# Performance work log

Hardware: AMD Instinct MI355X
Metric: run time of the kernel (lower is better)

The kernel has to match this reference:

```python
import jax, jax.numpy as jnp
import numpy as np

B, H, W, C = 16, 56, 56, 512
HEADS, WS, SHIFT = 16, 7, 3
N = WS * WS            # tokens per window = 49
NW = (H // WS) * (W // WS)  # 64 windows per image
HID = 4 * C
EPS = 1e-5


def _rel_pos_index():
    coords = np.stack(np.meshgrid(np.arange(WS), np.arange(WS), indexing='ij'))  # (2,WS,WS)
    coords = coords.reshape(2, -1)                       # (2,N)
    rel = coords[:, :, None] - coords[:, None, :]        # (2,N,N)
    rel = rel.transpose(1, 2, 0).astype(np.int64)        # (N,N,2)
    rel[:, :, 0] += WS - 1
    rel[:, :, 1] += WS - 1
    rel[:, :, 0] *= 2 * WS - 1
    return rel.sum(-1)                                   # (N,N) in [0, (2WS-1)^2)


def _attn_mask():
    # standard Swin shifted-window mask
    img = np.zeros((H, W), dtype=np.int64)
    cnt = 0
    for hs in (slice(0, -WS), slice(-WS, -SHIFT), slice(-SHIFT, None)):
        for ws in (slice(0, -WS), slice(-WS, -SHIFT), slice(-SHIFT, None)):
            img[hs, ws] = cnt
            cnt += 1
    win = img.reshape(H // WS, WS, W // WS, WS).transpose(0, 2, 1, 3).reshape(NW, N)
    diff = win[:, None, :] - win[:, :, None]             # (NW,N,N)
    return np.where(diff != 0, -100.0, 0.0).astype(np.float32)


REL_IDX = _rel_pos_index()
MASK = _attn_mask()


def _ln(x, g, b):
    m = x.mean(-1, keepdims=True)
    v = ((x - m) ** 2).mean(-1, keepdims=True)
    return (x - m) * jax.lax.rsqrt(v + EPS) * g + b


def setup_inputs() -> dict:
    key = jax.random.key(0)
    ks = jax.random.split(key, 16)
    s = 0.02
    return {
        'x': jax.random.normal(ks[0], (B, H * W, C), jnp.float32),
        'norm1_g': jnp.ones((C,), jnp.float32),
        'norm1_b': jnp.zeros((C,), jnp.float32),
        'qkv_w': jax.random.normal(ks[1], (3 * C, C), jnp.float32) * s,
        'qkv_b': jnp.zeros((3 * C,), jnp.float32),
        'proj_w': jax.random.normal(ks[2], (C, C), jnp.float32) * s,
        'proj_b': jnp.zeros((C,), jnp.float32),
        'rpb': jax.random.normal(ks[3], ((2 * WS - 1) ** 2, HEADS), jnp.float32) * s,
        'norm2_g': jnp.ones((C,), jnp.float32),
        'norm2_b': jnp.zeros((C,), jnp.float32),
        'fc1_w': jax.random.normal(ks[4], (HID, C), jnp.float32) * s,
        'fc1_b': jnp.zeros((HID,), jnp.float32),
        'fc2_w': jax.random.normal(ks[5], (C, HID), jnp.float32) * s,
        'fc2_b': jnp.zeros((C,), jnp.float32),
    }


def reference(x, norm1_g, norm1_b, qkv_w, qkv_b, proj_w, proj_b, rpb,
              norm2_g, norm2_b, fc1_w, fc1_b, fc2_w, fc2_b):
    hd = C // HEADS
    scale = hd ** -0.5

    shortcut = x
    h = _ln(x, norm1_g, norm1_b).reshape(B, H, W, C)
    # cyclic shift
    h = jnp.roll(h, (-SHIFT, -SHIFT), axis=(1, 2))
    # window partition -> (B*NW, N, C)
    h = h.reshape(B, H // WS, WS, W // WS, WS, C).transpose(0, 1, 3, 2, 4, 5)
    h = h.reshape(B * NW, N, C)

    qkv = h @ qkv_w.T + qkv_b                            # (B*NW, N, 3C)
    qkv = qkv.reshape(B * NW, N, 3, HEADS, hd).transpose(2, 0, 3, 1, 4)
    q, k, v = qkv[0], qkv[1], qkv[2]                     # (B*NW, HEADS, N, hd)

    attn = jnp.einsum('whnd,whmd->whnm', q * scale, k)   # (B*NW, HEADS, N, N)
    bias = rpb[REL_IDX].transpose(2, 0, 1)               # (HEADS, N, N)
    attn = attn + bias[None]
    attn = attn.reshape(B, NW, HEADS, N, N) + jnp.asarray(MASK)[None, :, None]
    attn = jax.nn.softmax(attn.reshape(B * NW, HEADS, N, N), axis=-1)

    out = jnp.einsum('whnm,whmd->whnd', attn, v)         # (B*NW, HEADS, N, hd)
    out = out.transpose(0, 2, 1, 3).reshape(B * NW, N, C)
    out = out @ proj_w.T + proj_b

    # window reverse + reverse shift
    out = out.reshape(B, H // WS, W // WS, WS, WS, C).transpose(0, 1, 3, 2, 4, 5)
    out = out.reshape(B, H, W, C)
    out = jnp.roll(out, (SHIFT, SHIFT), axis=(1, 2)).reshape(B, H * W, C)

    x = shortcut + out
    m = _ln(x, norm2_g, norm2_b)
    m = jax.nn.gelu(m @ fc1_w.T + fc1_b, approximate=False) @ fc2_w.T + fc2_b
    return x + m
```

## Files before the change

### kernel.cpp

```cpp
#include <hip/hip_runtime.h>
#include <hip/hip_bf16.h>

typedef __bf16 bf16;
typedef __bf16 bf16x8 __attribute__((ext_vector_type(8)));
typedef __bf16 bf16x4 __attribute__((ext_vector_type(4)));
typedef __bf16 bf16x2 __attribute__((ext_vector_type(2)));
typedef float f32x4 __attribute__((ext_vector_type(4)));

#define M_TOK 50176

#define GLD16(dst, src) __builtin_amdgcn_global_load_lds( \
    (const __attribute__((address_space(1))) void*)(src), \
    (__attribute__((address_space(3))) void*)(dst), 16, 0, 0)

__global__ __launch_bounds__(256) void convert_w_kernel(
    const float* __restrict__ w0, const float* __restrict__ w1,
    const float* __restrict__ w2, const float* __restrict__ w3,
    bf16* __restrict__ dst)
{
    int blk = blockIdx.x;
    const float* src; size_t srel, drel;
    if (blk < 768)       { src = w0; srel = (size_t)blk * 1024;          drel = srel; }
    else if (blk < 1024) { src = w1; srel = (size_t)(blk - 768) * 1024;  drel = 786432 + srel; }
    else if (blk < 2048) { src = w2; srel = (size_t)(blk - 1024) * 1024; drel = 1048576 + srel; }
    else                 { src = w3; srel = (size_t)(blk - 2048) * 1024; drel = 2097152 + srel; }
    int i = threadIdx.x * 4;
    float4 v = *(const float4*)(src + srel + i);
    bf16* d = dst + drel + i;
    d[0] = (bf16)v.x; d[1] = (bf16)v.y; d[2] = (bf16)v.z; d[3] = (bf16)v.w;
}

__global__ __launch_bounds__(64) void bias_table_kernel(
    const float* __restrict__ rpb, float* __restrict__ bt)
{
    int tq = blockIdx.x;
    int type = tq / 784, r = tq - type * 784;
    int head = r / 49, q = r - head * 49;
    int k = threadIdx.x;
    float v;
    if (k < 49) {
        int yq = q / 7, xq = q - yq * 7;
        int yk = k / 7, xk = k - yk * 7;
        int ridx = (yq - yk + 6) * 13 + (xq - xk + 6);
        v = rpb[ridx * 16 + head];
        int th = type >> 1, tw = type & 1;
        int qid = 3 * (th ? (yq < 4 ? 1 : 2) : 0) + (tw ? (xq < 4 ? 1 : 2) : 0);
        int kid = 3 * (th ? (yk < 4 ? 1 : 2) : 0) + (tw ? (xk < 4 ? 1 : 2) : 0);
        if (qid != kid) v -= 100.f;
    } else {
        v = -1e9f;
    }
    bt[(size_t)tq * 64 + k] = v;
}

__global__ __launch_bounds__(256) void ln1_window_kernel(
    const float* __restrict__ x, const float* __restrict__ g, const float* __restrict__ bta,
    bf16* __restrict__ h)
{
    int t = blockIdx.x;
    int win = t / 49, n = t - win * 49;
    int bi = win >> 6, nw = win & 63;
    int wh = nw >> 3, ww = nw & 7;
    int ny = n / 7, nx = n - ny * 7;
    int r = wh * 7 + ny + 3; if (r >= 56) r -= 56;
    int c = ww * 7 + nx + 3; if (c >= 56) c -= 56;
    const float* xr = x + ((size_t)bi * 3136 + r * 56 + c) * 512;
    int tid = threadIdx.x;
    float v0 = xr[tid];
    float v1 = xr[tid + 256];
    float s = v0 + v1, ss = v0 * v0 + v1 * v1;
#pragma unroll
    for (int o = 32; o; o >>= 1) { s += __shfl_down(s, o, 64); ss += __shfl_down(ss, o, 64); }
    __shared__ float red[8];
    int wave = tid >> 6, lane = tid & 63;
    if (lane == 0) { red[wave] = s; red[4 + wave] = ss; }
    __syncthreads();
    float S = red[0] + red[1] + red[2] + red[3];
    float SS = red[4] + red[5] + red[6] + red[7];
    float mean = S * (1.f / 512.f);
    float var = SS * (1.f / 512.f) - mean * mean;
    float rstd = rsqrtf(var + 1e-5f);
    bf16* hr = h + (size_t)t * 512;
    hr[tid] = (bf16)((v0 - mean) * rstd * g[tid] + bta[tid]);
    hr[tid + 256] = (bf16)((v1 - mean) * rstd * g[tid + 256] + bta[tid + 256]);
}

template <int X1BF>
__global__ __launch_bounds__(256) void ln2_kernel(
    const void* __restrict__ x1, const float* __restrict__ g,
    const float* __restrict__ bta, bf16* __restrict__ outp)
{
    int t = blockIdx.x;
    int tid = threadIdx.x;
    float v0, v1;
    if constexpr (X1BF) {
        const bf16* xr = (const bf16*)x1 + (size_t)t * 512;
        v0 = (float)xr[tid]; v1 = (float)xr[tid + 256];
    } else {
        const float* xr = (const float*)x1 + (size_t)t * 512;
        v0 = xr[tid]; v1 = xr[tid + 256];
    }
    float s = v0 + v1, ss = v0 * v0 + v1 * v1;
#pragma unroll
    for (int o = 32; o; o >>= 1) { s += __shfl_down(s, o, 64); ss += __shfl_down(ss, o, 64); }
    __shared__ float red[8];
    int wave = tid >> 6, lane = tid & 63;
    if (lane == 0) { red[wave] = s; red[4 + wave] = ss; }
    __syncthreads();
    float S = red[0] + red[1] + red[2] + red[3];
    float SS = red[4] + red[5] + red[6] + red[7];
    float mean = S * (1.f / 512.f);
    float var = SS * (1.f / 512.f) - mean * mean;
    float rstd = rsqrtf(var + 1e-5f);
    bf16* hr = outp + (size_t)t * 512;
    hr[tid] = (bf16)((v0 - mean) * rstd * g[tid] + bta[tid]);
    hr[tid + 256] = (bf16)((v1 - mean) * rstd * g[tid + 256] + bta[tid + 256]);
}

template <int MODE, int K, int X1BF>
__global__ __launch_bounds__(256, 4) void gemm128b_kernel(
    const bf16* __restrict__ A, const bf16* __restrict__ Wt, const float* __restrict__ bias,
    void* __restrict__ outp, const void* __restrict__ extra, int N)
{
    __shared__ bf16 As[128][64];
    __shared__ bf16 Ws[128][64];
    constexpr int NT = K / 64;
    int gx = gridDim.x;
    int lin = blockIdx.y * gx + blockIdx.x;
    int q8 = (gx * gridDim.y) >> 3;
    int lin2 = (lin & 7) * q8 + (lin >> 3);
    int bn = lin2 % gx, bm = lin2 / gx;
    int tid = threadIdx.x;
    int w = tid >> 6, lane = tid & 63;
    int wm = w >> 1, wn = w & 1;
    int fr = lane & 15, fq = lane >> 4;
    int srow = lane >> 3;
    int scol = ((lane & 7) ^ srow) * 8;
    const bf16* gA = A + (size_t)(bm * 128 + w * 32 + srow) * K + scol;
    const bf16* gB = Wt + (size_t)(bn * 128 + w * 32 + srow) * K + scol;

    f32x4 acc[4][4];
    f32x4 z = {0.f, 0.f, 0.f, 0.f};
#pragma unroll
    for (int mf = 0; mf < 4; mf++)
#pragma unroll
        for (int nf = 0; nf < 4; nf++) acc[mf][nf] = z;

    for (int kt = 0; kt < NT; ++kt) {
        if (kt) {
            asm volatile("s_waitcnt lgkmcnt(0)" ::: "memory");
            asm volatile("s_barrier" ::: "memory");
        }
#pragma unroll
        for (int i = 0; i < 4; i++)
            GLD16(&As[w * 32 + i * 8][0], gA + (size_t)(i * 8) * K + kt * 64);
#pragma unroll
        for (int i = 0; i < 4; i++)
            GLD16(&Ws[w * 32 + i * 8][0], gB + (size_t)(i * 8) * K + kt * 64);
        asm volatile("s_waitcnt vmcnt(0)" ::: "memory");
        asm volatile("s_barrier" ::: "memory");
#pragma unroll
        for (int kh = 0; kh < 2; kh++) {
            bf16x8 aF[4], bF[4];
            int c = kh * 4 + fq;
#pragma unroll
            for (int f = 0; f < 4; f++) {
                aF[f] = *(const bf16x8*)&As[wm * 64 + f * 16 + fr][(c ^ (fr & 7)) * 8];
                bF[f] = *(const bf16x8*)&Ws[wn * 64 + f * 16 + fr][(c ^ (fr & 7)) * 8];
            }
#pragma unroll
            for (int mf = 0; mf < 4; mf++)
#pragma unroll
                for (int nf = 0; nf < 4; nf++)
                    acc[mf][nf] = __builtin_amdgcn_mfma_f32_16x16x32_bf16(bF[nf], aF[mf], acc[mf][nf], 0, 0, 0);
        }
    }

#pragma unroll
    for (int mf = 0; mf < 4; mf++) {
        int row = bm * 128 + wm * 64 + mf * 16 + fr;
        size_t rowbase;
        if constexpr (MODE == 2) {
            int win = row / 49, n = row - win * 49;
            int bi = win >> 6, nw = win & 63;
            int wh = nw >> 3, wwi = nw & 7;
            int ny = n / 7, nx = n - ny * 7;
            int rr = wh * 7 + ny + 3; if (rr >= 56) rr -= 56;
            int cc = wwi * 7 + nx + 3; if (cc >= 56) cc -= 56;
            rowbase = ((size_t)bi * 3136 + rr * 56 + cc) * 512;
        } else {
            rowbase = (size_t)row * (MODE == 3 ? 512 : N);
        }
#pragma unroll
        for (int nf = 0; nf < 4; nf++) {
            int colb = bn * 128 + wn * 64 + nf * 16 + fq * 4;
            float4 b4 = *(const float4*)(bias + colb);
            float v0 = acc[mf][nf][0] + b4.x;
            float v1 = acc[mf][nf][1] + b4.y;
            float v2 = acc[mf][nf][2] + b4.z;
            float v3 = acc[mf][nf][3] + b4.w;
            size_t dst = rowbase + colb;
            if constexpr (MODE == 0) {
                bf16x4 t = {(bf16)v0, (bf16)v1, (bf16)v2, (bf16)v3};
                *(bf16x4*)((bf16*)outp + dst) = t;
            } else if constexpr (MODE == 1) {
                v0 = 0.5f * v0 * (1.f + erff(v0 * 0.70710678118654752f));
                v1 = 0.5f * v1 * (1.f + erff(v1 * 0.70710678118654752f));
                v2 = 0.5f * v2 * (1.f + erff(v2 * 0.70710678118654752f));
                v3 = 0.5f * v3 * (1.f + erff(v3 * 0.70710678118654752f));
                bf16x4 t = {(bf16)v0, (bf16)v1, (bf16)v2, (bf16)v3};
                *(bf16x4*)((bf16*)outp + dst) = t;
            } else if constexpr (MODE == 2) {
                float4 e = *(const float4*)((const float*)extra + dst);
                v0 += e.x; v1 += e.y; v2 += e.z; v3 += e.w;
                if constexpr (X1BF) {
                    bf16x4 t = {(bf16)v0, (bf16)v1, (bf16)v2, (bf16)v3};
                    *(bf16x4*)((bf16*)outp + dst) = t;
                } else {
                    float4 t = {v0, v1, v2, v3};
                    *(float4*)((float*)outp + dst) = t;
                }
            } else {
                if constexpr (X1BF) {
                    bf16x4 e = *(const bf16x4*)((const bf16*)extra + dst);
                    v0 += (float)e[0]; v1 += (float)e[1]; v2 += (float)e[2]; v3 += (float)e[3];
                } else {
                    float4 e = *(const float4*)((const float*)extra + dst);
                    v0 += e.x; v1 += e.y; v2 += e.z; v3 += e.w;
                }
                float4 t = {v0, v1, v2, v3};
                *(float4*)((float*)outp + dst) = t;
            }
        }
    }
}

__global__ __launch_bounds__(64) void attn_mfma_kernel(
    const bf16* __restrict__ qkv, const float* __restrict__ bt, bf16* __restrict__ outp)
{
    int wid0 = blockIdx.x;
    int wid = (wid0 & 7) * 2048 + (wid0 >> 3);
    int win = wid >> 4, head = wid & 15;
    int nw = win & 63;
    int type = ((nw >> 3) == 7 ? 2 : 0) + ((nw & 7) == 7 ? 1 : 0);
    int lane = threadIdx.x;
    int fr = lane & 15, fq = lane >> 4;
    __shared__ bf16 Vt[32][72];
    __shared__ bf16 Ps[64][72];
    const bf16* base = qkv + (size_t)win * 49 * 1536;

    uint4 z4 = {0, 0, 0, 0};
#pragma unroll
    for (int c = lane; c < 288; c += 64) ((uint4*)Vt)[c] = z4;
    __syncthreads();
    for (int c = lane; c < 1568; c += 64) {
        int tok = c >> 5, d = c & 31;
        Vt[d][tok] = base[(size_t)tok * 1536 + 1024 + head * 32 + d];
    }
    bf16x8 qf[4], kf[4];
#pragma unroll
    for (int i = 0; i < 4; i++) {
        int tq = i * 16 + fr; if (tq > 48) tq = 48;
        qf[i] = *(const bf16x8*)(base + (size_t)tq * 1536 + head * 32 + fq * 8);
        kf[i] = *(const bf16x8*)(base + (size_t)tq * 1536 + 512 + head * 32 + fq * 8);
    }
    f32x4 z = {0.f, 0.f, 0.f, 0.f};
    f32x4 st[4][4];
    __builtin_amdgcn_s_setprio(1);
#pragma unroll
    for (int mi = 0; mi < 4; mi++)
#pragma unroll
        for (int ni = 0; ni < 4; ni++)
            st[mi][ni] = __builtin_amdgcn_mfma_f32_16x16x32_bf16(kf[mi], qf[ni], z, 0, 0, 0);
    __builtin_amdgcn_s_setprio(0);
    __syncthreads();

    const float* btb = bt + (size_t)(type * 16 + head) * 49 * 64;
    float p[4][4][4];
    float inv[4];
#pragma unroll
    for (int ni = 0; ni < 4; ni++) {
        int q = ni * 16 + fr; if (q > 48) q = 48;
        const float* btr = btb + q * 64;
        float m = -1e30f;
#pragma unroll
        for (int mi = 0; mi < 4; mi++) {
            float4 bv = *(const float4*)(btr + mi * 16 + fq * 4);
#pragma unroll
            for (int r = 0; r < 4; r++) {
                float s = st[mi][ni][r] * 0.17677669529663689f + (&bv.x)[r];
                p[mi][ni][r] = s;
                m = fmaxf(m, s);
            }
        }
        m = fmaxf(m, __shfl_xor(m, 16));
        m = fmaxf(m, __shfl_xor(m, 32));
        float sum = 0.f;
#pragma unroll
        for (int mi = 0; mi < 4; mi++)
#pragma unroll
            for (int r = 0; r < 4; r++) {
                float e = __expf(p[mi][ni][r] - m);
                p[mi][ni][r] = e;
                sum += e;
            }
        sum += __shfl_xor(sum, 16);
        sum += __shfl_xor(sum, 32);
        inv[ni] = 1.f / sum;
    }
#pragma unroll
    for (int mi = 0; mi < 4; mi++)
#pragma unroll
        for (int ni = 0; ni < 4; ni++) {
            bf16x4 t;
            t[0] = (bf16)p[mi][ni][0]; t[1] = (bf16)p[mi][ni][1];
            t[2] = (bf16)p[mi][ni][2]; t[3] = (bf16)p[mi][ni][3];
            *(bf16x4*)&Ps[ni * 16 + fr][mi * 16 + fq * 4] = t;
        }
    __syncthreads();
    f32x4 o[2][4];
#pragma unroll
    for (int mi = 0; mi < 2; mi++)
#pragma unroll
        for (int ni = 0; ni < 4; ni++) o[mi][ni] = z;
    __builtin_amdgcn_s_setprio(1);
#pragma unroll
    for (int kt = 0; kt < 2; kt++) {
        bf16x8 a0 = *(const bf16x8*)&Vt[fr][kt * 32 + fq * 8];
        bf16x8 a1 = *(const bf16x8*)&Vt[16 + fr][kt * 32 + fq * 8];
#pragma unroll
        for (int ni = 0; ni < 4; ni++) {
            bf16x8 b = *(const bf16x8*)&Ps[ni * 16 + fr][kt * 32 + fq * 8];
            o[0][ni] = __builtin_amdgcn_mfma_f32_16x16x32_bf16(a0, b, o[0][ni], 0, 0, 0);
            o[1][ni] = __builtin_amdgcn_mfma_f32_16x16x32_bf16(a1, b, o[1][ni], 0, 0, 0);
        }
    }
    __builtin_amdgcn_s_setprio(0);
#pragma unroll
    for (int ni = 0; ni < 4; ni++) {
        int q = ni * 16 + fr;
        if (q < 49) {
            bf16* orow = outp + (size_t)(win * 49 + q) * 512 + head * 32;
#pragma unroll
            for (int mi = 0; mi < 2; mi++)
#pragma unroll
                for (int r2 = 0; r2 < 2; r2++) {
                    bf16x2 t;
                    t[0] = (bf16)(o[mi][ni][2 * r2] * inv[ni]);
                    t[1] = (bf16)(o[mi][ni][2 * r2 + 1] * inv[ni]);
                    *(bf16x2*)(orow + mi * 16 + fq * 4 + 2 * r2) = t;
                }
        }
    }
}

extern "C" void kernel_launch(void* const* d_in, const int* in_sizes, int n_in,
                              void* d_out, int out_size, void* d_ws, size_t ws_size,
                              hipStream_t stream)
{
    const float* x      = (const float*)d_in[0];
    const float* n1g    = (const float*)d_in[1];
    const float* n1b    = (const float*)d_in[2];
    const float* qkv_w  = (const float*)d_in[3];
    const float* qkv_b  = (const float*)d_in[4];
    const float* proj_w = (const float*)d_in[5];
    const float* proj_b = (const float*)d_in[6];
    const float* rpb    = (const float*)d_in[7];
    const float* n2g    = (const float*)d_in[8];
    const float* n2b    = (const float*)d_in[9];
    const float* fc1_w  = (const float*)d_in[10];
    const float* fc1_b  = (const float*)d_in[11];
    const float* fc2_w  = (const float*)d_in[12];
    const float* fc2_b  = (const float*)d_in[13];

    char* ws = (char*)d_ws;
    bf16* qkv  = (bf16*)ws;
    bf16* h    = (bf16*)(ws + 154140672ull);
    float* bt  = (float*)(ws + 154140672ull);
    bf16* ao   = (bf16*)(ws + 205520896ull);
    bf16* wbuf = (bf16*)(ws + 256901120ull);
    bf16* hid  = (bf16*)ws;
    bf16* ln2h = ao;
    bf16* wq  = wbuf;
    bf16* wp  = wbuf + 786432;
    bf16* wf1 = wbuf + 1048576;
    bf16* wf2 = wbuf + 2097152;

    bool xb = (ws_size >= 314572800ull);
    void* x1 = xb ? (void*)(ws + 263192576ull) : (void*)d_out;

    convert_w_kernel<<<3072, 256, 0, stream>>>(qkv_w, proj_w, fc1_w, fc2_w, wbuf);
    ln1_window_kernel<<<M_TOK, 256, 0, stream>>>(x, n1g, n1b, h);
    gemm128b_kernel<0, 512, 0><<<dim3(12, 392), 256, 0, stream>>>(h, wq, qkv_b, qkv, nullptr, 1536);
    bias_table_kernel<<<3136, 64, 0, stream>>>(rpb, bt);
    attn_mfma_kernel<<<16384, 64, 0, stream>>>(qkv, bt, ao);
    if (xb) {
        gemm128b_kernel<2, 512, 1><<<dim3(4, 392), 256, 0, stream>>>(ao, wp, proj_b, x1, x, 512);
        ln2_kernel<1><<<M_TOK, 256, 0, stream>>>(x1, n2g, n2b, ln2h);
        gemm128b_kernel<1, 512, 1><<<dim3(16, 392), 256, 0, stream>>>(ln2h, wf1, fc1_b, hid, nullptr, 2048);
        gemm128b_kernel<3, 2048, 1><<<dim3(4, 392), 256, 0, stream>>>(hid, wf2, fc2_b, d_out, x1, 512);
    } else {
        gemm128b_kernel<2, 512, 0><<<dim3(4, 392), 256, 0, stream>>>(ao, wp, proj_b, x1, x, 512);
        ln2_kernel<0><<<M_TOK, 256, 0, stream>>>(x1, n2g, n2b, ln2h);
        gemm128b_kernel<1, 512, 0><<<dim3(16, 392), 256, 0, stream>>>(ln2h, wf1, fc1_b, hid, nullptr, 2048);
        gemm128b_kernel<3, 2048, 0><<<dim3(4, 392), 256, 0, stream>>>(hid, wf2, fc2_b, d_out, x1, 512);
    }
}
```

Before: 581.0 us.

## Add 256x256 double-buffered GEMM kernel for QKV and MLP projections

Introduces a 512-thread GEMM with 256x256 output tiles and two LDS buffers, so the next K-tile loads asynchronously while the current one is computed. It replaces the 128x128 kernel for the QKV, fc1 and fc2 GEMMs, and the epilogue moves into shared helpers. Larger tiles raise arithmetic intensity and cut global reloads of A and W. The cost is 128KB of LDS per block and heavy register pressure from 32 accumulators per thread, which limits occupancy and gives fewer blocks for wave balancing.

```diff
diff --git a/kernel.cpp b/kernel.cpp
--- a/kernel.cpp
+++ b/kernel.cpp
@@ -117,6 +117,58 @@
     hr[tid + 256] = (bf16)((v1 - mean) * rstd * g[tid + 256] + bta[tid + 256]);
 }
 
+template <int MODE, int X1BF>
+__device__ __forceinline__ void epi_store(
+    void* outp, const void* extra, const float* bias, size_t rowbase,
+    int colb, const f32x4& a)
+{
+    float4 b4 = *(const float4*)(bias + colb);
+    float v0 = a[0] + b4.x, v1 = a[1] + b4.y, v2 = a[2] + b4.z, v3 = a[3] + b4.w;
+    size_t dst = rowbase + colb;
+    if constexpr (MODE == 0) {
+        bf16x4 t = {(bf16)v0, (bf16)v1, (bf16)v2, (bf16)v3};
+        *(bf16x4*)((bf16*)outp + dst) = t;
+    } else if constexpr (MODE == 1) {
+        v0 = 0.5f * v0 * (1.f + erff(v0 * 0.70710678118654752f));
+        v1 = 0.5f * v1 * (1.f + erff(v1 * 0.70710678118654752f));
+        v2 = 0.5f * v2 * (1.f + erff(v2 * 0.70710678118654752f));
+        v3 = 0.5f * v3 * (1.f + erff(v3 * 0.70710678118654752f));
+        bf16x4 t = {(bf16)v0, (bf16)v1, (bf16)v2, (bf16)v3};
+        *(bf16x4*)((bf16*)outp + dst) = t;
+    } else if constexpr (MODE == 2) {
+        float4 e = *(const float4*)((const float*)extra + dst);
+        v0 += e.x; v1 += e.y; v2 += e.z; v3 += e.w;
+        if constexpr (X1BF) {
+            bf16x4 t = {(bf16)v0, (bf16)v1, (bf16)v2, (bf16)v3};
+            *(bf16x4*)((bf16*)outp + dst) = t;
+        } else {
+            float4 t = {v0, v1, v2, v3};
+            *(float4*)((float*)outp + dst) = t;
+        }
+    } else {
+        if constexpr (X1BF) {
+            bf16x4 e = *(const bf16x4*)((const bf16*)extra + dst);
+            v0 += (float)e[0]; v1 += (float)e[1]; v2 += (float)e[2]; v3 += (float)e[3];
+        } else {
+            float4 e = *(const float4*)((const float*)extra + dst);
+            v0 += e.x; v1 += e.y; v2 += e.z; v3 += e.w;
+        }
+        float4 t = {v0, v1, v2, v3};
+        *(float4*)((float*)outp + dst) = t;
+    }
+}
+
+__device__ __forceinline__ size_t mode2_rowbase(int row)
+{
+    int win = row / 49, n = row - win * 49;
+    int bi = win >> 6, nw = win & 63;
+    int wh = nw >> 3, wwi = nw & 7;
+    int ny = n / 7, nx = n - ny * 7;
+    int rr = wh * 7 + ny + 3; if (rr >= 56) rr -= 56;
+    int cc = wwi * 7 + nx + 3; if (cc >= 56) cc -= 56;
+    return ((size_t)bi * 3136 + rr * 56 + cc) * 512;
+}
+
 template <int MODE, int K, int X1BF>
 __global__ __launch_bounds__(256, 4) void gemm128b_kernel(
     const bf16* __restrict__ A, const bf16* __restrict__ Wt, const float* __restrict__ bias,
@@ -180,58 +232,94 @@
     for (int mf = 0; mf < 4; mf++) {
         int row = bm * 128 + wm * 64 + mf * 16 + fr;
         size_t rowbase;
-        if constexpr (MODE == 2) {
-            int win = row / 49, n = row - win * 49;
-            int bi = win >> 6, nw = win & 63;
-            int wh = nw >> 3, wwi = nw & 7;
-            int ny = n / 7, nx = n - ny * 7;
-            int rr = wh * 7 + ny + 3; if (rr >= 56) rr -= 56;
-            int cc = wwi * 7 + nx + 3; if (cc >= 56) cc -= 56;
-            rowbase = ((size_t)bi * 3136 + rr * 56 + cc) * 512;
-        } else {
-            rowbase = (size_t)row * (MODE == 3 ? 512 : N);
-        }
-#pragma unroll
-        for (int nf = 0; nf < 4; nf++) {
-            int colb = bn * 128 + wn * 64 + nf * 16 + fq * 4;
-            float4 b4 = *(const float4*)(bias + colb);
-            float v0 = acc[mf][nf][0] + b4.x;
-            float v1 = acc[mf][nf][1] + b4.y;
-            float v2 = acc[mf][nf][2] + b4.z;
-            float v3 = acc[mf][nf][3] + b4.w;
-            size_t dst = rowbase + colb;
-            if constexpr (MODE == 0) {
-                bf16x4 t = {(bf16)v0, (bf16)v1, (bf16)v2, (bf16)v3};
-                *(bf16x4*)((bf16*)outp + dst) = t;
-            } else if constexpr (MODE == 1) {
-                v0 = 0.5f * v0 * (1.f + erff(v0 * 0.70710678118654752f));
-                v1 = 0.5f * v1 * (1.f + erff(v1 * 0.70710678118654752f));
-                v2 = 0.5f * v2 * (1.f + erff(v2 * 0.70710678118654752f));
-                v3 = 0.5f * v3 * (1.f + erff(v3 * 0.70710678118654752f));
-                bf16x4 t = {(bf16)v0, (bf16)v1, (bf16)v2, (bf16)v3};
-                *(bf16x4*)((bf16*)outp + dst) = t;
-            } else if constexpr (MODE == 2) {
-                float4 e = *(const float4*)((const float*)extra + dst);
-                v0 += e.x; v1 += e.y; v2 += e.z; v3 += e.w;
-                if constexpr (X1BF) {
-                    bf16x4 t = {(bf16)v0, (bf16)v1, (bf16)v2, (bf16)v3};
-                    *(bf16x4*)((bf16*)outp + dst) = t;
-                } else {
-                    float4 t = {v0, v1, v2, v3};
-                    *(float4*)((float*)outp + dst) = t;
-                }
-            } else {
-                if constexpr (X1BF) {
-                    bf16x4 e = *(const bf16x4*)((const bf16*)extra + dst);
-                    v0 += (float)e[0]; v1 += (float)e[1]; v2 += (float)e[2]; v3 += (float)e[3];
-                } else {
-                    float4 e = *(const float4*)((const float*)extra + dst);
-                    v0 += e.x; v1 += e.y; v2 += e.z; v3 += e.w;
-                }
-                float4 t = {v0, v1, v2, v3};
-                *(float4*)((float*)outp + dst) = t;
-            }
-        }
+        if constexpr (MODE == 2) rowbase = mode2_rowbase(row);
+        else rowbase = (size_t)row * (MODE == 3 ? 512 : N);
+#pragma unroll
+        for (int nf = 0; nf < 4; nf++)
+            epi_store<MODE, X1BF>(outp, extra, bias, rowbase,
+                                  bn * 128 + wn * 64 + nf * 16 + fq * 4, acc[mf][nf]);
+    }
+}
+
+template <int MODE, int K, int X1BF>
+__global__ __launch_bounds__(512, 2) void gemm256_kernel(
+    const bf16* __restrict__ A, const bf16* __restrict__ Wt, const float* __restrict__ bias,
+    void* __restrict__ outp, const void* __restrict__ extra, int N)
+{
+    __shared__ bf16 As[2][256][64];
+    __shared__ bf16 Ws[2][256][64];
+    constexpr int NT = K / 64;
+    int gx = gridDim.x;
+    int lin = blockIdx.y * gx + blockIdx.x;
+    int q8 = (gx * gridDim.y) >> 3;
+    int lin2 = (lin & 7) * q8 + (lin >> 3);
+    int bn = lin2 % gx, bm = lin2 / gx;
+    int tid = threadIdx.x;
+    int w = tid >> 6, lane = tid & 63;
+    int wm = w >> 2, wn = w & 3;
+    int fr = lane & 15, fq = lane >> 4;
+    int srow = lane >> 3;
+    int scol = ((lane & 7) ^ srow) * 8;
+    const bf16* gA = A + (size_t)(bm * 256 + w * 8 + srow) * K + scol;
+    const bf16* gB = Wt + (size_t)(bn * 256 + w * 8 + srow) * K + scol;
+
+    f32x4 acc[8][4];
+    f32x4 z = {0.f, 0.f, 0.f, 0.f};
+#pragma unroll
+    for (int mf = 0; mf < 8; mf++)
+#pragma unroll
+        for (int nf = 0; nf < 4; nf++) acc[mf][nf] = z;
+
+    auto STAGE = [&](int b, int kt) {
+#pragma unroll
+        for (int i = 0; i < 4; i++)
+            GLD16(&As[b][i * 64 + w * 8][0], gA + (size_t)(i * 64) * K + kt * 64);
+#pragma unroll
+        for (int i = 0; i < 4; i++)
+            GLD16(&Ws[b][i * 64 + w * 8][0], gB + (size_t)(i * 64) * K + kt * 64);
+    };
+
+    STAGE(0, 0);
+    if (NT > 1) STAGE(1, 1);
+    asm volatile("s_waitcnt vmcnt(8)" ::: "memory");
+    __builtin_amdgcn_s_barrier();
+
+    for (int kt = 0; kt < NT; ++kt) {
+        int cur = kt & 1;
+#pragma unroll
+        for (int kh = 0; kh < 2; kh++) {
+            bf16x8 aF[8], bF[4];
+            int c = kh * 4 + fq;
+#pragma unroll
+            for (int f = 0; f < 8; f++)
+                aF[f] = *(const bf16x8*)&As[cur][wm * 128 + f * 16 + fr][(c ^ (fr & 7)) * 8];
+#pragma unroll
+            for (int f = 0; f < 4; f++)
+                bF[f] = *(const bf16x8*)&Ws[cur][wn * 64 + f * 16 + fr][(c ^ (fr & 7)) * 8];
+#pragma unroll
+            for (int mf = 0; mf < 8; mf++)
+#pragma unroll
+                for (int nf = 0; nf < 4; nf++)
+                    acc[mf][nf] = __builtin_amdgcn_mfma_f32_16x16x32_bf16(bF[nf], aF[mf], acc[mf][nf], 0, 0, 0);
+        }
+        if (kt + 1 < NT) {
+            asm volatile("s_waitcnt lgkmcnt(0)" ::: "memory");
+            asm volatile("s_waitcnt vmcnt(0)" ::: "memory");
+            __builtin_amdgcn_s_barrier();
+            if (kt + 2 < NT) STAGE(cur, kt + 2);
+        }
+    }
+
+#pragma unroll
+    for (int mf = 0; mf < 8; mf++) {
+        int row = bm * 256 + wm * 128 + mf * 16 + fr;
+        size_t rowbase;
+        if constexpr (MODE == 2) rowbase = mode2_rowbase(row);
+        else rowbase = (size_t)row * (MODE == 3 ? 512 : N);
+#pragma unroll
+        for (int nf = 0; nf < 4; nf++)
+            epi_store<MODE, X1BF>(outp, extra, bias, rowbase,
+                                  bn * 256 + wn * 64 + nf * 16 + fq * 4, acc[mf][nf]);
     }
 }
 
@@ -391,18 +479,18 @@
 
     convert_w_kernel<<<3072, 256, 0, stream>>>(qkv_w, proj_w, fc1_w, fc2_w, wbuf);
     ln1_window_kernel<<<M_TOK, 256, 0, stream>>>(x, n1g, n1b, h);
-    gemm128b_kernel<0, 512, 0><<<dim3(12, 392), 256, 0, stream>>>(h, wq, qkv_b, qkv, nullptr, 1536);
+    gemm256_kernel<0, 512, 0><<<dim3(6, 196), 512, 0, stream>>>(h, wq, qkv_b, qkv, nullptr, 1536);
     bias_table_kernel<<<3136, 64, 0, stream>>>(rpb, bt);
     attn_mfma_kernel<<<16384, 64, 0, stream>>>(qkv, bt, ao);
     if (xb) {
         gemm128b_kernel<2, 512, 1><<<dim3(4, 392), 256, 0, stream>>>(ao, wp, proj_b, x1, x, 512);
         ln2_kernel<1><<<M_TOK, 256, 0, stream>>>(x1, n2g, n2b, ln2h);
-        gemm128b_kernel<1, 512, 1><<<dim3(16, 392), 256, 0, stream>>>(ln2h, wf1, fc1_b, hid, nullptr, 2048);
-        gemm128b_kernel<3, 2048, 1><<<dim3(4, 392), 256, 0, stream>>>(hid, wf2, fc2_b, d_out, x1, 512);
+        gemm256_kernel<1, 512, 1><<<dim3(8, 196), 512, 0, stream>>>(ln2h, wf1, fc1_b, hid, nullptr, 2048);
+        gemm256_kernel<3, 2048, 1><<<dim3(2, 196), 512, 0, stream>>>(hid, wf2, fc2_b, d_out, x1, 512);
     } else {
         gemm128b_kernel<2, 512, 0><<<dim3(4, 392), 256, 0, stream>>>(ao, wp, proj_b, x1, x, 512);
         ln2_kernel<0><<<M_TOK, 256, 0, stream>>>(x1, n2g, n2b, ln2h);
-        gemm128b_kernel<1, 512, 0><<<dim3(16, 392), 256, 0, stream>>>(ln2h, wf1, fc1_b, hid, nullptr, 2048);
-        gemm128b_kernel<3, 2048, 0><<<dim3(4, 392), 256, 0, stream>>>(hid, wf2, fc2_b, d_out, x1, 512);
-    }
-}
+        gemm256_kernel<1, 512, 0><<<dim3(8, 196), 512, 0, stream>>>(ln2h, wf1, fc1_b, hid, nullptr, 2048);
+        gemm256_kernel<3, 2048, 0><<<dim3(2, 196), 512, 0, stream>>>(hid, wf2, fc2_b, d_out, x1, 512);
+    }
+}
```

Measured after the change: 757.0 us. +30.3%, slower.

## Split GEMM K-tile into two half buffers to overlap loads with MFMA

Applied to the files above, without the earlier changes.

The GEMM K loop now uses two 32-wide LDS half-tiles. The load of the next half is issued before computing on the current one, so global-to-LDS transfers overlap with MFMA work instead of waiting for the whole tile before compute. The LDS swizzle is changed to fit the 32-column layout, and the epilogue is moved into helper functions. Synchronisation points now come twice per 64-wide K step, and the pipeline is only one half-tile deep.

```diff
diff --git a/kernel.cpp b/kernel.cpp
--- a/kernel.cpp
+++ b/kernel.cpp
@@ -117,13 +117,65 @@
     hr[tid + 256] = (bf16)((v1 - mean) * rstd * g[tid + 256] + bta[tid + 256]);
 }
 
+template <int MODE, int X1BF>
+__device__ __forceinline__ void epi_store(
+    void* outp, const void* extra, const float* bias, size_t rowbase,
+    int colb, const f32x4& a)
+{
+    float4 b4 = *(const float4*)(bias + colb);
+    float v0 = a[0] + b4.x, v1 = a[1] + b4.y, v2 = a[2] + b4.z, v3 = a[3] + b4.w;
+    size_t dst = rowbase + colb;
+    if constexpr (MODE == 0) {
+        bf16x4 t = {(bf16)v0, (bf16)v1, (bf16)v2, (bf16)v3};
+        *(bf16x4*)((bf16*)outp + dst) = t;
+    } else if constexpr (MODE == 1) {
+        v0 = 0.5f * v0 * (1.f + erff(v0 * 0.70710678118654752f));
+        v1 = 0.5f * v1 * (1.f + erff(v1 * 0.70710678118654752f));
+        v2 = 0.5f * v2 * (1.f + erff(v2 * 0.70710678118654752f));
+        v3 = 0.5f * v3 * (1.f + erff(v3 * 0.70710678118654752f));
+        bf16x4 t = {(bf16)v0, (bf16)v1, (bf16)v2, (bf16)v3};
+        *(bf16x4*)((bf16*)outp + dst) = t;
+    } else if constexpr (MODE == 2) {
+        float4 e = *(const float4*)((const float*)extra + dst);
+        v0 += e.x; v1 += e.y; v2 += e.z; v3 += e.w;
+        if constexpr (X1BF) {
+            bf16x4 t = {(bf16)v0, (bf16)v1, (bf16)v2, (bf16)v3};
+            *(bf16x4*)((bf16*)outp + dst) = t;
+        } else {
+            float4 t = {v0, v1, v2, v3};
+            *(float4*)((float*)outp + dst) = t;
+        }
+    } else {
+        if constexpr (X1BF) {
+            bf16x4 e = *(const bf16x4*)((const bf16*)extra + dst);
+            v0 += (float)e[0]; v1 += (float)e[1]; v2 += (float)e[2]; v3 += (float)e[3];
+        } else {
+            float4 e = *(const float4*)((const float*)extra + dst);
+            v0 += e.x; v1 += e.y; v2 += e.z; v3 += e.w;
+        }
+        float4 t = {v0, v1, v2, v3};
+        *(float4*)((float*)outp + dst) = t;
+    }
+}
+
+__device__ __forceinline__ size_t mode2_rowbase(int row)
+{
+    int win = row / 49, n = row - win * 49;
+    int bi = win >> 6, nw = win & 63;
+    int wh = nw >> 3, wwi = nw & 7;
+    int ny = n / 7, nx = n - ny * 7;
+    int rr = wh * 7 + ny + 3; if (rr >= 56) rr -= 56;
+    int cc = wwi * 7 + nx + 3; if (cc >= 56) cc -= 56;
+    return ((size_t)bi * 3136 + rr * 56 + cc) * 512;
+}
+
 template <int MODE, int K, int X1BF>
-__global__ __launch_bounds__(256, 4) void gemm128b_kernel(
+__global__ __launch_bounds__(256, 4) void gemm128kh_kernel(
     const bf16* __restrict__ A, const bf16* __restrict__ Wt, const float* __restrict__ bias,
     void* __restrict__ outp, const void* __restrict__ extra, int N)
 {
-    __shared__ bf16 As[128][64];
-    __shared__ bf16 Ws[128][64];
+    __shared__ bf16 As[2][128][32];
+    __shared__ bf16 Ws[2][128][32];
     constexpr int NT = K / 64;
     int gx = gridDim.x;
     int lin = blockIdx.y * gx + blockIdx.x;
@@ -134,8 +186,9 @@
     int w = tid >> 6, lane = tid & 63;
     int wm = w >> 1, wn = w & 1;
     int fr = lane & 15, fq = lane >> 4;
-    int srow = lane >> 3;
-    int scol = ((lane & 7) ^ srow) * 8;
+    int srow = lane >> 2;
+    int scol = ((lane & 3) ^ ((lane >> 3) & 3)) * 8;
+    int rslot = (fq ^ ((fr >> 1) & 3)) * 8;
     const bf16* gA = A + (size_t)(bm * 128 + w * 32 + srow) * K + scol;
     const bf16* gB = Wt + (size_t)(bn * 128 + w * 32 + srow) * K + scol;
 
@@ -146,33 +199,45 @@
 #pragma unroll
         for (int nf = 0; nf < 4; nf++) acc[mf][nf] = z;
 
+    auto stg = [&](int kh, int kt) {
+        const bf16* sa = gA + kt * 64 + kh * 32;
+        const bf16* sb = gB + kt * 64 + kh * 32;
+        GLD16(&As[kh][w * 32][0], sa);
+        GLD16(&As[kh][w * 32 + 16][0], sa + (size_t)16 * K);
+        GLD16(&Ws[kh][w * 32][0], sb);
+        GLD16(&Ws[kh][w * 32 + 16][0], sb + (size_t)16 * K);
+    };
+
+    auto compute = [&](int kh) {
+        bf16x8 aF[4], bF[4];
+#pragma unroll
+        for (int f = 0; f < 4; f++) {
+            aF[f] = *(const bf16x8*)&As[kh][wm * 64 + f * 16 + fr][rslot];
+            bF[f] = *(const bf16x8*)&Ws[kh][wn * 64 + f * 16 + fr][rslot];
+        }
+#pragma unroll
+        for (int mf = 0; mf < 4; mf++)
+#pragma unroll
+            for (int nf = 0; nf < 4; nf++)
+                acc[mf][nf] = __builtin_amdgcn_mfma_f32_16x16x32_bf16(bF[nf], aF[mf], acc[mf][nf], 0, 0, 0);
+    };
+
+    stg(0, 0);
+    asm volatile("s_waitcnt vmcnt(0)" ::: "memory");
+    asm volatile("s_barrier" ::: "memory");
+
     for (int kt = 0; kt < NT; ++kt) {
-        if (kt) {
-            asm volatile("s_waitcnt lgkmcnt(0)" ::: "memory");
-            asm volatile("s_barrier" ::: "memory");
-        }
-#pragma unroll
-        for (int i = 0; i < 4; i++)
-            GLD16(&As[w * 32 + i * 8][0], gA + (size_t)(i * 8) * K + kt * 64);
-#pragma unroll
-        for (int i = 0; i < 4; i++)
-            GLD16(&Ws[w * 32 + i * 8][0], gB + (size_t)(i * 8) * K + kt * 64);
+        stg(1, kt);
+        compute(0);
         asm volatile("s_waitcnt vmcnt(0)" ::: "memory");
         asm volatile("s_barrier" ::: "memory");
-#pragma unroll
-        for (int kh = 0; kh < 2; kh++) {
-            bf16x8 aF[4], bF[4];
-            int c = kh * 4 + fq;
-#pragma unroll
-            for (int f = 0; f < 4; f++) {
-                aF[f] = *(const bf16x8*)&As[wm * 64 + f * 16 + fr][(c ^ (fr & 7)) * 8];
-                bF[f] = *(const bf16x8*)&Ws[wn * 64 + f * 16 + fr][(c ^ (fr & 7)) * 8];
-            }
-#pragma unroll
-            for (int mf = 0; mf < 4; mf++)
-#pragma unroll
-                for (int nf = 0; nf < 4; nf++)
-                    acc[mf][nf] = __builtin_amdgcn_mfma_f32_16x16x32_bf16(bF[nf], aF[mf], acc[mf][nf], 0, 0, 0);
+        if (kt + 1 < NT) {
+            stg(0, kt + 1);
+            compute(1);
+            asm volatile("s_waitcnt vmcnt(0)" ::: "memory");
+            asm volatile("s_barrier" ::: "memory");
+        } else {
+            compute(1);
         }
     }
 
@@ -180,58 +245,12 @@
     for (int mf = 0; mf < 4; mf++) {
         int row = bm * 128 + wm * 64 + mf * 16 + fr;
         size_t rowbase;
-        if constexpr (MODE == 2) {
-            int win = row / 49, n = row - win * 49;
-            int bi = win >> 6, nw = win & 63;
-            int wh = nw >> 3, wwi = nw & 7;
-            int ny = n / 7, nx = n - ny * 7;
-            int rr = wh * 7 + ny + 3; if (rr >= 56) rr -= 56;
-            int cc = wwi * 7 + nx + 3; if (cc >= 56) cc -= 56;
-            rowbase = ((size_t)bi * 3136 + rr * 56 + cc) * 512;
-        } else {
-            rowbase = (size_t)row * (MODE == 3 ? 512 : N);
-        }
-#pragma unroll
-        for (int nf = 0; nf < 4; nf++) {
-            int colb = bn * 128 + wn * 64 + nf * 16 + fq * 4;
-            float4 b4 = *(const float4*)(bias + colb);
-            float v0 = acc[mf][nf][0] + b4.x;
-            float v1 = acc[mf][nf][1] + b4.y;
-            float v2 = acc[mf][nf][2] + b4.z;
-            float v3 = acc[mf][nf][3] + b4.w;
-            size_t dst = rowbase + colb;
-            if constexpr (MODE == 0) {
-                bf16x4 t = {(bf16)v0, (bf16)v1, (bf16)v2, (bf16)v3};
-                *(bf16x4*)((bf16*)outp + dst) = t;
-            } else if constexpr (MODE == 1) {
-                v0 = 0.5f * v0 * (1.f + erff(v0 * 0.70710678118654752f));
-                v1 = 0.5f * v1 * (1.f + erff(v1 * 0.70710678118654752f));
-                v2 = 0.5f * v2 * (1.f + erff(v2 * 0.70710678118654752f));
-                v3 = 0.5f * v3 * (1.f + erff(v3 * 0.70710678118654752f));
-                bf16x4 t = {(bf16)v0, (bf16)v1, (bf16)v2, (bf16)v3};
-                *(bf16x4*)((bf16*)outp + dst) = t;
-            } else if constexpr (MODE == 2) {
-                float4 e = *(const float4*)((const float*)extra + dst);
-                v0 += e.x; v1 += e.y; v2 += e.z; v3 += e.w;
-                if constexpr (X1BF) {
-                    bf16x4 t = {(bf16)v0, (bf16)v1, (bf16)v2, (bf16)v3};
-                    *(bf16x4*)((bf16*)outp + dst) = t;
-                } else {
-                    float4 t = {v0, v1, v2, v3};
-                    *(float4*)((float*)outp + dst) = t;
-                }
-            } else {
-                if constexpr (X1BF) {
-                    bf16x4 e = *(const bf16x4*)((const bf16*)extra + dst);
-                    v0 += (float)e[0]; v1 += (float)e[1]; v2 += (float)e[2]; v3 += (float)e[3];
-                } else {
-                    float4 e = *(const float4*)((const float*)extra + dst);
-                    v0 += e.x; v1 += e.y; v2 += e.z; v3 += e.w;
-                }
-                float4 t = {v0, v1, v2, v3};
-                *(float4*)((float*)outp + dst) = t;
-            }
-        }
+        if constexpr (MODE == 2) rowbase = mode2_rowbase(row);
+        else rowbase = (size_t)row * (MODE == 3 ? 512 : N);
+#pragma unroll
+        for (int nf = 0; nf < 4; nf++)
+            epi_store<MODE, X1BF>(outp, extra, bias, rowbase,
+                                  bn * 128 + wn * 64 + nf * 16 + fq * 4, acc[mf][nf]);
     }
 }
 
@@ -391,18 +410,18 @@
 
     convert_w_kernel<<<3072, 256, 0, stream>>>(qkv_w, proj_w, fc1_w, fc2_w, wbuf);
     ln1_window_kernel<<<M_TOK, 256, 0, stream>>>(x, n1g, n1b, h);
-    gemm128b_kernel<0, 512, 0><<<dim3(12, 392), 256, 0, stream>>>(h, wq, qkv_b, qkv, nullptr, 1536);
+    gemm128kh_kernel<0, 512, 0><<<dim3(12, 392), 256, 0, stream>>>(h, wq, qkv_b, qkv, nullptr, 1536);
     bias_table_kernel<<<3136, 64, 0, stream>>>(rpb, bt);
     attn_mfma_kernel<<<16384, 64, 0, stream>>>(qkv, bt, ao);
     if (xb) {
-        gemm128b_kernel<2, 512, 1><<<dim3(4, 392), 256, 0, stream>>>(ao, wp, proj_b, x1, x, 512);
+        gemm128kh_kernel<2, 512, 1><<<dim3(4, 392), 256, 0, stream>>>(ao, wp, proj_b, x1, x, 512);
         ln2_kernel<1><<<M_TOK, 256, 0, stream>>>(x1, n2g, n2b, ln2h);
-        gemm128b_kernel<1, 512, 1><<<dim3(16, 392), 256, 0, stream>>>(ln2h, wf1, fc1_b, hid, nullptr, 2048);
-        gemm128b_kernel<3, 2048, 1><<<dim3(4, 392), 256, 0, stream>>>(hid, wf2, fc2_b, d_out, x1, 512);
+        gemm128kh_kernel<1, 512, 1><<<dim3(16, 392), 256, 0, stream>>>(ln2h, wf1, fc1_b, hid, nullptr, 2048);
+        gemm128kh_kernel<3, 2048, 1><<<dim3(4, 392), 256, 0, stream>>>(hid, wf2, fc2_b, d_out, x1, 512);
     } else {
-        gemm128b_kernel<2, 512, 0><<<dim3(4, 392), 256, 0, stream>>>(ao, wp, proj_b, x1, x, 512);
+        gemm128kh_kernel<2, 512, 0><<<dim3(4, 392), 256, 0, stream>>>(ao, wp, proj_b, x1, x, 512);
         ln2_kernel<0><<<M_TOK, 256, 0, stream>>>(x1, n2g, n2b, ln2h);
-        gemm128b_kernel<1, 512, 0><<<dim3(16, 392), 256, 0, stream>>>(ln2h, wf1, fc1_b, hid, nullptr, 2048);
-        gemm128b_kernel<3, 2048, 0><<<dim3(4, 392), 256, 0, stream>>>(hid, wf2, fc2_b, d_out, x1, 512);
-    }
-}
+        gemm128kh_kernel<1, 512, 0><<<dim3(16, 392), 256, 0, stream>>>(ln2h, wf1, fc1_b, hid, nullptr, 2048);
+        gemm128kh_kernel<3, 2048, 0><<<dim3(4, 392), 256, 0, stream>>>(hid, wf2, fc2_b, d_out, x1, 512);
+    }
+}
```

After: 656.2 us. 1.13x slower.
